# Kernel tuning notes

Hardware: AMD Instinct MI355X
Metric: run time of the kernel (lower is better)

The kernel has to match this reference:

```python
import jax, jax.numpy as jnp
import numpy as np

D, NH, K, FF, S, B = 256, 4, 1024, 1024, 2048, 4  # nhead*d_model must equal key_feature_dim=1024


def _ln(x, g, b, eps=1e-5):
    m = jnp.mean(x, axis=-1, keepdims=True)
    v = jnp.mean((x - m) ** 2, axis=-1, keepdims=True)
    return (x - m) / jnp.sqrt(v + eps) * g + b


def _l2norm(x, eps=1e-12):  # F.normalize(p=2, dim=-1)
    n = jnp.sqrt(jnp.sum(x * x, axis=-1, keepdims=True))
    return x / jnp.maximum(n, eps)


def setup_inputs() -> dict:
    key = jax.random.key(0)
    ks = jax.random.split(key, 16)
    def rn(i, shape, s):
        return jax.random.normal(ks[i], shape, jnp.float32) * jnp.float32(s)
    z = lambda shape: jnp.zeros(shape, jnp.float32)
    o = lambda shape: jnp.ones(shape, jnp.float32)
    return {
        "srcc": jax.random.normal(ks[0], (S, B, D), jnp.float32),
        "memory": jax.random.normal(ks[1], (S, B, D), jnp.float32),
        # per-head RelationUnit weights (stacked over NH heads)
        "WK": rn(2, (NH, K, D), np.sqrt(2.0 / K)),
        "WQ": rn(3, (NH, K, D), np.sqrt(2.0 / K)),
        "WV": rn(4, (NH, D, D), np.sqrt(2.0 / D)),
        "Wt": rn(5, (NH, D, D), np.sqrt(1.0 / D)),   # trans_conv
        # per-head TransNonlinear (extra_nonlinear)
        "e1w": rn(6, (NH, K, D), np.sqrt(1.0 / D)), "e1b": z((NH, K)),
        "e2w": rn(7, (NH, D, K), np.sqrt(1.0 / K)), "e2b": z((NH, D)),
        "eg": o((NH, D)), "eb": z((NH, D)),
        "Wout": rn(8, (D, NH * D), np.sqrt(1.0 / (NH * D))),  # trans_conv_out
        # decoder-layer FFN + norms
        "l1w": rn(9, (FF, D), np.sqrt(1.0 / D)), "l1b": z((FF,)),
        "l2w": rn(10, (D, FF), np.sqrt(1.0 / FF)), "l2b": z((D,)),
        "n1g": o((D,)), "n1b": z((D,)),
        "n3g": o((D,)), "n3b": z((D,)),
    }


def _forward(srcc, memory, WK, WQ, WV, Wt, e1w, e1b, e2w, e2b, eg, eb,
             Wout, l1w, l1b, l2w, l2b, n1g, n1b, n3g, n3b):
    # RMA(query=memory, key=srcc, value=srcc); dropout = identity (eval mode)
    q, kv = memory, srcc  # [S,B,D]
    wk = _l2norm(jnp.einsum('sbd,hkd->hsbk', kv, WK))   # [h,S,B,K]
    wq = _l2norm(jnp.einsum('sbd,hkd->hsbk', q, WQ))
    dot = jnp.einsum('hqbk,hsbk->hbqs', wq, wk)          # [h,B,Sq,Sk]
    aff = jax.nn.softmax(dot, axis=-1)
    # custom renormalization over the *query* axis (torch dim=1 of [B,Sq,Sk])
    aff = aff / (1e-9 + jnp.sum(aff, axis=2, keepdims=True))
    wv = jnp.einsum('sbd,hed->hbse', kv, WV)             # [h,B,Sk,D]
    o = jnp.einsum('hbqs,hbse->hqbe', aff, wv)           # [h,Sq,B,D]
    ru = jax.nn.relu(jnp.einsum('hqbd,hed->hqbe', q[None] - o, Wt))
    # per-head TransNonlinear
    hmid = jax.nn.relu(jnp.einsum('hqbd,hkd->hqbk', ru, e1w) + e1b[:, None, None, :])
    s2 = jnp.einsum('hqbk,hdk->hqbd', hmid, e2w) + e2b[:, None, None, :]
    xh = _ln(ru + s2, eg[:, None, None, :], eb[:, None, None, :])  # [h,S,B,D]
    cat = jnp.moveaxis(xh, 0, 2).reshape(q.shape[0], q.shape[1], NH * D)  # concat heads
    rma_out = jnp.einsum('sbk,dk->sbd', cat, Wout)       # [S,B,D]
    # decoder layer: note the faithful `[0]` indexing from the source
    srcc2 = rma_out[0]                                    # [B,D]
    x = _ln(memory + srcc2[None, :, :], n1g, n1b)         # broadcast residual
    ff = jax.nn.relu(x @ l1w.T + l1b) @ l2w.T + l2b
    return _ln(x + ff, n3g, n3b)


def reference(srcc, memory, WK, WQ, WV, Wt, e1w, e1b, e2w, e2b, eg, eb,
              Wout, l1w, l1b, l2w, l2b, n1g, n1b, n3g, n3b):
    return _forward(srcc, memory, WK, WQ, WV, Wt, e1w, e1b, e2w, e2b, eg, eb,
                    Wout, l1w, l1b, l2w, l2b, n1g, n1b, n3g, n3b)
```

## Files before the change

### kernel.cpp

```cpp
#include <hip/hip_runtime.h>
#include <stdint.h>
#include <stdio.h>

#define S_  2048
#define B_  4
#define D_  256
#define NH_ 4
#define K_  1024
#define FF_ 1024
#define M_  (S_*B_)
#define HB_ (NH_*B_)

#define LDSROW 136
#define PROW 144

typedef float  f32x4  __attribute__((ext_vector_type(4)));
typedef __bf16 bf16x8 __attribute__((ext_vector_type(8)));

__device__ __forceinline__ float bf2f(unsigned short u) {
  union { unsigned int i; float f; } v; v.i = ((unsigned int)u) << 16; return v.f;
}
__device__ __forceinline__ unsigned short f2bf(float f) {
  union { float f; unsigned int i; } v; v.f = f;
  unsigned int r = v.i + 0x7fffu + ((v.i >> 16) & 1u);
  return (unsigned short)(r >> 16);
}
__device__ __forceinline__ unsigned char f2fp8(float f) {
  return (unsigned char)(__builtin_amdgcn_cvt_pk_fp8_f32(f, f, 0, false) & 0xff);
}

__device__ __forceinline__ int kperm(int k) {
  int ks = k >> 5, quad = (k >> 3) & 3, b = k & 7;
  return ((ks >> 1) << 6) + (quad << 4) + ((ks & 1) << 3) + b;
}

__device__ __forceinline__ void gld_lds16(const void* g, void* l) {
  __builtin_amdgcn_global_load_lds(
      (__attribute__((address_space(1))) void*)(uintptr_t)g,
      (__attribute__((address_space(3))) void*)(uintptr_t)l, 16, 0, 0);
}

__device__ __forceinline__ void gemm_kloop(
    const unsigned short* __restrict__ Ag, const unsigned short* __restrict__ Bg,
    int lda, int ldb, int kdim,
    unsigned short* __restrict__ smA, unsigned short* __restrict__ smB,
    f32x4 acc[4][4])
{
  const int t    = threadIdx.x;
  const int wave = t >> 6;
  const int lane = t & 63;
  const int wm   = (wave >> 1) << 6;
  const int wn   = (wave & 1) << 6;
  const int c16  = lane & 15;
  const int quad = lane >> 4;

  for (int kc = 0; kc < kdim; kc += 64) {
    __syncthreads();
#pragma unroll
    for (int it = 0; it < 4; ++it) {
      int c   = it*256 + t;
      int row = c >> 3;
      int g   = (c & 7) ^ (row & 7);
      const unsigned short* ga = Ag + (size_t)row*lda + kc + g*8;
      const unsigned short* gb = Bg + (size_t)row*ldb + kc + g*8;
      unsigned short* la = smA + (size_t)(it*256 + wave*64)*8;
      unsigned short* lb = smB + (size_t)(it*256 + wave*64)*8;
      gld_lds16(ga, la);
      gld_lds16(gb, lb);
    }
    asm volatile("s_waitcnt vmcnt(0)" ::: "memory");
    __syncthreads();
#pragma unroll
    for (int ks = 0; ks < 2; ++ks) {
      bf16x8 av[4], bv[4];
#pragma unroll
      for (int i = 0; i < 4; ++i) {
        int ra = wm + i*16 + c16;
        av[i] = *(const bf16x8*)(smA + ra*64 + (((ks*4 + quad) ^ (ra & 7)))*8);
        int rb = wn + i*16 + c16;
        bv[i] = *(const bf16x8*)(smB + rb*64 + (((ks*4 + quad) ^ (rb & 7)))*8);
      }
#pragma unroll
      for (int i = 0; i < 4; ++i)
#pragma unroll
        for (int j = 0; j < 4; ++j)
          acc[i][j] = __builtin_amdgcn_mfma_f32_16x16x32_bf16(av[i], bv[j], acc[i][j], 0, 0, 0);
    }
  }
}

__device__ __forceinline__ float blk_sum256(float v, float* red) {
#pragma unroll
  for (int o = 32; o; o >>= 1) v += __shfl_xor(v, o, 64);
  __syncthreads();
  if ((threadIdx.x & 63) == 0) red[threadIdx.x >> 6] = v;
  __syncthreads();
  return red[0] + red[1] + red[2] + red[3];
}

__device__ __forceinline__ float wave_red(float a) {
#pragma unroll
  for (int o = 1; o < 64; o <<= 1) a += __shfl_xor(a, o, 64);
  return a;
}

__global__ void __launch_bounds__(256) k_cvt6(
    const float* __restrict__ s0, unsigned short* __restrict__ d0,
    const float* __restrict__ s1, unsigned short* __restrict__ d1,
    const float* __restrict__ s2, unsigned short* __restrict__ d2,
    const float* __restrict__ s3, unsigned short* __restrict__ d3,
    const float* __restrict__ s4, unsigned short* __restrict__ d4,
    const float* __restrict__ s5, unsigned short* __restrict__ d5) {
  int b = blockIdx.x;
  const float* src; unsigned short* dst; int base;
  if      (b < 2048) { src = s0; dst = d0; base = b; }
  else if (b < 4096) { src = s1; dst = d1; base = b - 2048; }
  else if (b < 5120) { src = s2; dst = d2; base = b - 4096; }
  else if (b < 6144) { src = s3; dst = d3; base = b - 5120; }
  else if (b < 6400) { src = s4; dst = d4; base = b - 6144; }
  else               { src = s5; dst = d5; base = b - 6400; }
  int i = (base*256 + threadIdx.x)*4;
  float4 v = *(const float4*)(src + i);
  ushort4 o;
  o.x = f2bf(v.x); o.y = f2bf(v.y); o.z = f2bf(v.z); o.w = f2bf(v.w);
  *(ushort4*)(dst + i) = o;
}

__global__ void __launch_bounds__(256) k_proj2(
    const unsigned short* __restrict__ X0, const unsigned short* __restrict__ W0,
    float* __restrict__ n0p, unsigned char* __restrict__ o0p,
    const unsigned short* __restrict__ X1, const unsigned short* __restrict__ W1,
    float* __restrict__ n1p, unsigned char* __restrict__ o1p) {
  __shared__ __align__(16) unsigned short sm[128*LDSROW];
  int which = blockIdx.x >> 11;
  const unsigned short* X = which ? X1 : X0;
  const unsigned short* W = which ? W1 : W0;
  float* nsq = which ? n1p : n0p;
  unsigned char* outp = which ? o1p : o0p;
  int l = blockIdx.x & 2047, x = l & 7, rblk = l >> 3;
  int m0 = (rblk >> 2)*128;
  int n0 = (x*4 + (rblk & 3))*128;
  f32x4 acc[4][4];
#pragma unroll
  for (int i = 0; i < 4; ++i)
#pragma unroll
    for (int j = 0; j < 4; ++j) acc[i][j] = f32x4{0.f,0.f,0.f,0.f};
  gemm_kloop(X + (size_t)m0*D_, W + (size_t)n0*D_, D_, D_, D_, sm, sm + 128*64, acc);
  const int t = threadIdx.x, wave = t>>6, lane = t&63;
  const int wm = (wave>>1)*64, wn = (wave&1)*64, quad = lane>>4, c16 = lane&15;
  const int h = n0 >> 10;
  unsigned char* sm8 = (unsigned char*)sm;
  __syncthreads();
#pragma unroll
  for (int i = 0; i < 4; ++i)
#pragma unroll
    for (int r = 0; r < 4; ++r) {
      int mloc = wm + i*16 + quad*4 + r;
      float sq = 0.f;
#pragma unroll
      for (int j = 0; j < 4; ++j) {
        float v = acc[i][j][r];
        sm8[mloc*PROW + kperm(wn + j*16 + c16)] = f2fp8(v);
        sq += v*v;
      }
      sq += __shfl_xor(sq, 1, 64); sq += __shfl_xor(sq, 2, 64);
      sq += __shfl_xor(sq, 4, 64); sq += __shfl_xor(sq, 8, 64);
      if (c16 == 0) {
        int m = m0 + mloc;
        atomicAdd(&nsq[(size_t)(h*B_ + (m & 3))*S_ + (m >> 2)], sq);
      }
    }
  __syncthreads();
  const int cg = t & 7, rsub = t >> 3;
#pragma unroll
  for (int c = 0; c < 4; ++c) {
    int mloc = c*32 + rsub;
    int m = m0 + mloc, s = m >> 2, b = m & 3;
    uint4 val = *(const uint4*)(sm8 + mloc*PROW + cg*16);
    *(uint4*)(outp + ((size_t)(h*B_ + b)*S_ + s)*K_ + (n0 & (K_-1)) + cg*16) = val;
  }
}

__global__ void __launch_bounds__(256) k_qkA(const unsigned char* __restrict__ wqa,
    const unsigned char* __restrict__ wka, const float* __restrict__ nq,
    const float* __restrict__ nk, float* __restrict__ lrow,
    unsigned short* __restrict__ E) {
  __shared__ __align__(16) unsigned short sm[128*LDSROW];
  unsigned char* smA = (unsigned char*)sm;
  unsigned char* smB = smA + 128*128;
  int l = blockIdx.x, x = l & 7, rblk = l >> 3;
  int hb = rblk >> 5;
  int rr = rblk & 31;
  int q0 = (x*2 + (rr & 1))*128;
  int s0 = (rr >> 1)*128;
  const unsigned char* A  = wqa + (size_t)hb*S_*K_ + (size_t)q0*K_;
  const unsigned char* Bm = wka + (size_t)hb*S_*K_ + (size_t)s0*K_;
  const int t = threadIdx.x, wave = t>>6, lane = t&63;
  const int wm = (wave>>1)*64, wn = (wave&1)*64, quad = lane>>4, c16 = lane&15;
  f32x4 acc[4][4];
#pragma unroll
  for (int i = 0; i < 4; ++i)
#pragma unroll
    for (int j = 0; j < 4; ++j) acc[i][j] = f32x4{0.f,0.f,0.f,0.f};

  for (int kc = 0; kc < K_; kc += 128) {
    __syncthreads();
#pragma unroll
    for (int it = 0; it < 4; ++it) {
      int c   = it*256 + t;
      int row = c >> 3;
      int g   = (c & 7) ^ (row & 7);
      gld_lds16(A  + (size_t)row*K_ + kc + g*16, smA + (size_t)(it*256 + wave*64)*16);
      gld_lds16(Bm + (size_t)row*K_ + kc + g*16, smB + (size_t)(it*256 + wave*64)*16);
    }
    asm volatile("s_waitcnt vmcnt(0)" ::: "memory");
    __syncthreads();
#pragma unroll
    for (int j2 = 0; j2 < 2; ++j2) {
      uint4 a4[4], b4[4];
#pragma unroll
      for (int i = 0; i < 4; ++i) {
        int ra = wm + i*16 + c16;
        a4[i] = *(const uint4*)(smA + ra*128 + (((j2*4 + quad) ^ (ra & 7)))*16);
        int rb = wn + i*16 + c16;
        b4[i] = *(const uint4*)(smB + rb*128 + (((j2*4 + quad) ^ (rb & 7)))*16);
      }
#pragma unroll
      for (int hh = 0; hh < 2; ++hh)
#pragma unroll
        for (int i = 0; i < 4; ++i)
#pragma unroll
          for (int j = 0; j < 4; ++j)
            acc[i][j] = __builtin_amdgcn_mfma_f32_16x16x32_fp8_fp8(
                ((const long*)&a4[i])[hh], ((const long*)&b4[j])[hh],
                acc[i][j], 0, 0, 0);
    }
  }

  float rk4[4];
#pragma unroll
  for (int j = 0; j < 4; ++j)
    rk4[j] = rsqrtf(nk[(size_t)hb*S_ + s0 + wn + j*16 + c16]);
  __syncthreads();
#pragma unroll
  for (int i = 0; i < 4; ++i)
#pragma unroll
    for (int r = 0; r < 4; ++r) {
      int qloc = wm + i*16 + quad*4 + r;
      float rq = rsqrtf(nq[(size_t)hb*S_ + q0 + qloc]);
      float rs = 0.f;
#pragma unroll
      for (int j = 0; j < 4; ++j) {
        float e = __expf(acc[i][j][r] * rq * rk4[j]);
        rs += e;
        sm[qloc*LDSROW + wn + j*16 + c16] = f2bf(e);
      }
      rs += __shfl_xor(rs, 1, 64); rs += __shfl_xor(rs, 2, 64);
      rs += __shfl_xor(rs, 4, 64); rs += __shfl_xor(rs, 8, 64);
      if (c16 == 0) atomicAdd(&lrow[(size_t)hb*S_ + q0 + qloc], rs);
    }
  __syncthreads();
  const int col8 = (t & 15)*8, rsub = t >> 4;
#pragma unroll
  for (int c = 0; c < 8; ++c) {
    int qloc = c*16 + rsub;
    uint4 val = *(const uint4*)(sm + qloc*LDSROW + col8);
    *(uint4*)(E + ((size_t)hb*S_ + q0 + qloc)*S_ + s0 + col8) = val;
  }
}

__global__ void __launch_bounds__(256) k_colsumE(const unsigned short* __restrict__ E,
    const float* __restrict__ lrow, float* __restrict__ colsum,
    float* __restrict__ p0) {
  __shared__ float il[128];
  int hb = blockIdx.x, qc = blockIdx.y;
  int t  = threadIdx.x;
  if (t < 128) il[t] = 1.f / lrow[(size_t)hb*S_ + qc*128 + t];
  __syncthreads();
  const unsigned short* Eb = E + (size_t)hb*S_*S_ + (size_t)(qc*128)*S_ + t*8;
  float acc8[8] = {0,0,0,0,0,0,0,0};
  for (int qi = 0; qi < 128; ++qi) {
    uint4 u = *(const uint4*)(Eb + (size_t)qi*S_);
    float w = il[qi];
    unsigned int ws_[4] = {u.x, u.y, u.z, u.w};
    float v8[8];
#pragma unroll
    for (int k = 0; k < 4; ++k) {
      v8[2*k]   = bf2f((unsigned short)(ws_[k] & 0xffffu));
      v8[2*k+1] = bf2f((unsigned short)(ws_[k] >> 16));
    }
#pragma unroll
    for (int k = 0; k < 8; ++k) acc8[k] += v8[k] * w;
    if (qc == 0 && qi == 0) {
#pragma unroll
      for (int k = 0; k < 8; ++k) p0[(size_t)hb*S_ + t*8 + k] = v8[k] * w;
    }
  }
#pragma unroll
  for (int k = 0; k < 8; ++k)
    atomicAdd(&colsum[(size_t)hb*S_ + t*8 + k], acc8[k]);
}

__global__ void __launch_bounds__(256) k_mid0(const float* __restrict__ p0,
    const float* __restrict__ colsum, const float* __restrict__ kv,
    float* __restrict__ cbuf) {
  __shared__ float aff[128];
  int hb = blockIdx.x, sc = blockIdx.y;
  int b = hb & 3;
  int t = threadIdx.x;
  if (t < 128) {
    int s = sc*128 + t;
    aff[t] = p0[(size_t)hb*S_ + s] / (1e-9f + colsum[(size_t)hb*S_ + s]);
  }
  __syncthreads();
  float acc = 0.f;
#pragma unroll 4
  for (int i = 0; i < 128; ++i) {
    int s = sc*128 + i;
    acc += aff[i] * kv[((size_t)s*B_ + b)*D_ + t];
  }
  atomicAdd(&cbuf[hb*D_ + t], acc);
}

__global__ void __launch_bounds__(256) k_mid1a(const float* __restrict__ cbuf,
    const float* __restrict__ mem, const float* __restrict__ WV,
    const float* __restrict__ Wt, float* __restrict__ ruW) {
  __shared__ float cS[D_], qmo[D_];
  int hb = blockIdx.x, h = hb >> 2, b = hb & 3;
  int t = threadIdx.x, wave = t >> 6, lane = t & 63;
  cS[t] = cbuf[hb*D_ + t];
  __syncthreads();
  float4 cv = *(const float4*)(cS + lane*4);
  for (int rr = 0; rr < 64; ++rr) {
    int e = wave*64 + rr;
    float4 w = *(const float4*)(WV + ((size_t)h*D_ + e)*D_ + lane*4);
    float a = wave_red(cv.x*w.x + cv.y*w.y + cv.z*w.z + cv.w*w.w);
    if (lane == 0) qmo[e] = mem[(size_t)b*D_ + e] - a;
  }
  __syncthreads();
  float4 qv = *(const float4*)(qmo + lane*4);
  for (int rr = 0; rr < 64; ++rr) {
    int e = wave*64 + rr;
    float4 w = *(const float4*)(Wt + ((size_t)h*D_ + e)*D_ + lane*4);
    float a = wave_red(qv.x*w.x + qv.y*w.y + qv.z*w.z + qv.w*w.w);
    if (lane == 0) ruW[hb*D_ + e] = fmaxf(a, 0.f);
  }
}

__global__ void __launch_bounds__(256) k_mid1b(const float* __restrict__ ruW,
    const float* __restrict__ e1w, const float* __restrict__ e1b,
    float* __restrict__ hmW) {
  __shared__ float ru[D_];
  int hb = blockIdx.x, kc = blockIdx.y, h = hb >> 2;
  int t = threadIdx.x, wave = t >> 6, lane = t & 63;
  ru[t] = ruW[hb*D_ + t];
  __syncthreads();
  float4 rv = *(const float4*)(ru + lane*4);
  for (int rr = 0; rr < 32; ++rr) {
    int k = kc*128 + wave*32 + rr;
    float4 w = *(const float4*)(e1w + ((size_t)h*K_ + k)*D_ + lane*4);
    float a = wave_red(rv.x*w.x + rv.y*w.y + rv.z*w.z + rv.w*w.w);
    if (lane == 0) hmW[hb*K_ + k] = fmaxf(a + e1b[(size_t)h*K_ + k], 0.f);
  }
}

__global__ void __launch_bounds__(256) k_mid1c(const float* __restrict__ hmW,
    const float* __restrict__ e2w, const float* __restrict__ e2b,
    float* __restrict__ s2W) {
  __shared__ float hm[K_];
  int hb = blockIdx.x, dc = blockIdx.y, h = hb >> 2;
  int t = threadIdx.x, wave = t >> 6, lane = t & 63;
  for (int k = t; k < K_; k += 256) hm[k] = hmW[hb*K_ + k];
  __syncthreads();
  for (int rr = 0; rr < 8; ++rr) {
    int d = dc*32 + wave*8 + rr;
    const float* row = e2w + ((size_t)h*D_ + d)*K_;
    float a = 0.f;
#pragma unroll
    for (int p = 0; p < 4; ++p) {
      float4 w = *(const float4*)(row + (p*64 + lane)*4);
      float4 hv = *(const float4*)(hm + (p*64 + lane)*4);
      a += w.x*hv.x + w.y*hv.y + w.z*hv.z + w.w*hv.w;
    }
    a = wave_red(a);
    if (lane == 0) s2W[hb*D_ + d] = a + e2b[(size_t)h*D_ + d];
  }
}

__global__ void __launch_bounds__(256) k_mid1d(const float* __restrict__ ruW,
    const float* __restrict__ s2W, const float* __restrict__ eg,
    const float* __restrict__ ebias, float* __restrict__ xh0) {
  __shared__ float red[4];
  int hb = blockIdx.x, h = hb >> 2;
  int t = threadIdx.x;
  float tv = ruW[hb*D_ + t] + s2W[hb*D_ + t];
  float mean = blk_sum256(tv, red) * (1.f/D_);
  float dv = tv - mean;
  float var = blk_sum256(dv*dv, red) * (1.f/D_);
  xh0[hb*D_ + t] = dv * rsqrtf(var + 1e-5f) * eg[(size_t)h*D_ + t] + ebias[(size_t)h*D_ + t];
}

__global__ void __launch_bounds__(256) k_mid2(const float* __restrict__ xh0,
    const float* __restrict__ Wout, float* __restrict__ srcc2) {
  __shared__ float cat[NH_*D_];
  int b = blockIdx.x, dc = blockIdx.y;
  int t = threadIdx.x, wave = t >> 6, lane = t & 63;
  for (int n = t; n < NH_*D_; n += 256)
    cat[n] = xh0[((size_t)(n >> 8)*B_ + b)*D_ + (n & 255)];
  __syncthreads();
  for (int rr = 0; rr < 8; ++rr) {
    int d = dc*32 + wave*8 + rr;
    const float* row = Wout + (size_t)d*(NH_*D_);
    float a = 0.f;
#pragma unroll
    for (int p = 0; p < 4; ++p) {
      float4 w = *(const float4*)(row + (p*64 + lane)*4);
      float4 cv = *(const float4*)(cat + (p*64 + lane)*4);
      a += w.x*cv.x + w.y*cv.y + w.z*cv.z + w.w*cv.w;
    }
    a = wave_red(a);
    if (lane == 0) srcc2[b*D_ + d] = a;
  }
}

__global__ void __launch_bounds__(256) k_f1(const float* __restrict__ mem,
    const float* __restrict__ srcc2, const float* __restrict__ g,
    const float* __restrict__ bb, float* __restrict__ xf,
    unsigned short* __restrict__ xb) {
  __shared__ float red[4];
  int m = blockIdx.x, t = threadIdx.x;
  float v = mem[(size_t)m*D_ + t] + srcc2[(m & 3)*D_ + t];
  float mean = blk_sum256(v, red) * (1.f/D_);
  float d = v - mean;
  float var = blk_sum256(d*d, red) * (1.f/D_);
  float y = d * rsqrtf(var + 1e-5f) * g[t] + bb[t];
  xf[(size_t)m*D_ + t] = y;
  xb[(size_t)m*D_ + t] = f2bf(y);
}

__global__ void __launch_bounds__(256) k_f2(const unsigned short* __restrict__ xb,
    const unsigned short* __restrict__ l1wb, const float* __restrict__ l1b,
    unsigned short* __restrict__ h1) {
  __shared__ __align__(16) unsigned short sm[128*LDSROW];
  int l = blockIdx.x;
  int n0 = (l & 7)*128, m0 = (l >> 3)*128;
  f32x4 acc[4][4];
#pragma unroll
  for (int i = 0; i < 4; ++i)
#pragma unroll
    for (int j = 0; j < 4; ++j) acc[i][j] = f32x4{0.f,0.f,0.f,0.f};
  gemm_kloop(xb + (size_t)m0*D_, l1wb + (size_t)n0*D_, D_, D_, D_, sm, sm + 128*64, acc);
  const int t = threadIdx.x, wave = t>>6, lane = t&63;
  const int wm = (wave>>1)*64, wn = (wave&1)*64, quad = lane>>4, c16 = lane&15;
  __syncthreads();
#pragma unroll
  for (int i = 0; i < 4; ++i)
#pragma unroll
    for (int r = 0; r < 4; ++r) {
      int mloc = wm + i*16 + quad*4 + r;
#pragma unroll
      for (int j = 0; j < 4; ++j) {
        int n = n0 + wn + j*16 + c16;
        sm[mloc*LDSROW + wn + j*16 + c16] = f2bf(fmaxf(acc[i][j][r] + l1b[n], 0.f));
      }
    }
  __syncthreads();
  const int col8 = (t & 15)*8, rsub = t >> 4;
#pragma unroll
  for (int c = 0; c < 8; ++c) {
    int mloc = c*16 + rsub;
    uint4 val = *(const uint4*)(sm + mloc*LDSROW + col8);
    *(uint4*)(h1 + (size_t)(m0 + mloc)*FF_ + n0 + col8) = val;
  }
}

__global__ void __launch_bounds__(256) k_f3(const unsigned short* __restrict__ h1,
    const unsigned short* __restrict__ l2wb, float* __restrict__ yf) {
  __shared__ __align__(16) unsigned short smA[128*64], smB[128*64];
  int l = blockIdx.x;
  int z = l & 1, n0 = ((l >> 1) & 1)*128, m0 = (l >> 2)*128;
  f32x4 acc[4][4];
#pragma unroll
  for (int i = 0; i < 4; ++i)
#pragma unroll
    for (int j = 0; j < 4; ++j) acc[i][j] = f32x4{0.f,0.f,0.f,0.f};
  gemm_kloop(h1 + (size_t)m0*FF_ + z*512, l2wb + (size_t)n0*FF_ + z*512,
             FF_, FF_, 512, smA, smB, acc);
  const int t = threadIdx.x, wave = t>>6, lane = t&63;
  const int wm = (wave>>1)*64, wn = (wave&1)*64, quad = lane>>4, c16 = lane&15;
#pragma unroll
  for (int i = 0; i < 4; ++i)
#pragma unroll
    for (int r = 0; r < 4; ++r) {
      int m = m0 + wm + i*16 + quad*4 + r;
#pragma unroll
      for (int j = 0; j < 4; ++j) {
        int n = n0 + wn + j*16 + c16;
        atomicAdd(&yf[(size_t)m*D_ + n], acc[i][j][r]);
      }
    }
}

__global__ void __launch_bounds__(256) k_f4(const float* __restrict__ yf,
    const float* __restrict__ l2b, const float* __restrict__ xf,
    const float* __restrict__ g, const float* __restrict__ bb,
    float* __restrict__ out) {
  __shared__ float red[4];
  int m = blockIdx.x, t = threadIdx.x;
  float v = yf[(size_t)m*D_ + t] + l2b[t] + xf[(size_t)m*D_ + t];
  float mean = blk_sum256(v, red) * (1.f/D_);
  float d = v - mean;
  float var = blk_sum256(d*d, red) * (1.f/D_);
  out[(size_t)m*D_ + t] = d * rsqrtf(var + 1e-5f) * g[t] + bb[t];
}

constexpr size_t SZ_ACT  = (size_t)HB_*S_*K_;
constexpr size_t OFF_WQA = 0;
constexpr size_t OFF_WKA = OFF_WQA + SZ_ACT;
constexpr size_t OFF_KVB = OFF_WKA + SZ_ACT;
constexpr size_t OFF_QB  = OFF_KVB + (size_t)M_*D_*2;
constexpr size_t OFF_WKW = OFF_QB  + (size_t)M_*D_*2;
constexpr size_t OFF_WQW = OFF_WKW + (size_t)NH_*K_*D_*2;
constexpr size_t OFF_L1W = OFF_WQW + (size_t)NH_*K_*D_*2;
constexpr size_t OFF_L2W = OFF_L1W + (size_t)FF_*D_*2;
constexpr size_t OFF_XB  = OFF_L2W + (size_t)D_*FF_*2;
constexpr size_t OFF_H1  = OFF_XB  + (size_t)M_*D_*2;
constexpr size_t OFF_XF  = OFF_H1  + (size_t)M_*FF_*2;
constexpr size_t OFF_YF  = OFF_XF  + (size_t)M_*D_*4;
constexpr size_t OFF_NQ  = OFF_YF  + (size_t)M_*D_*4;
constexpr size_t OFF_NK  = OFF_NQ + (size_t)HB_*S_*4;
constexpr size_t OFF_L   = OFF_NK + (size_t)HB_*S_*4;
constexpr size_t OFF_CS  = OFF_L  + (size_t)HB_*S_*4;
constexpr size_t OFF_CB  = OFF_CS + (size_t)HB_*S_*4;
constexpr size_t ZERO_BYTES = (size_t)HB_*S_*4*4 + (size_t)HB_*D_*4;
constexpr size_t OFF_P0  = OFF_CB + (size_t)HB_*D_*4;
constexpr size_t OFF_XH0 = OFF_P0 + (size_t)HB_*S_*4;
constexpr size_t OFF_SC2 = OFF_XH0 + (size_t)HB_*D_*4;
constexpr size_t OFF_RU  = OFF_SC2 + (size_t)B_*D_*4;
constexpr size_t OFF_HM  = OFF_RU  + (size_t)HB_*D_*4;
constexpr size_t OFF_S2  = OFF_HM  + (size_t)HB_*K_*4;
constexpr size_t OFF_E   = OFF_S2  + (size_t)HB_*D_*4;
constexpr size_t SZ_E    = (size_t)HB_*S_*S_*2;
constexpr size_t NEED_ALL = OFF_E + SZ_E;

extern "C" void kernel_launch(void* const* d_in, const int* in_sizes, int n_in,
                              void* d_out, int out_size, void* d_ws, size_t ws_size,
                              hipStream_t stream) {
  (void)in_sizes; (void)out_size;
  if (n_in < 21) return;
  const float* srcc = (const float*)d_in[0];
  const float* mem  = (const float*)d_in[1];
  const float* WK   = (const float*)d_in[2];
  const float* WQ   = (const float*)d_in[3];
  const float* WV   = (const float*)d_in[4];
  const float* Wt   = (const float*)d_in[5];
  const float* e1w  = (const float*)d_in[6];
  const float* e1b  = (const float*)d_in[7];
  const float* e2w  = (const float*)d_in[8];
  const float* e2b  = (const float*)d_in[9];
  const float* eg   = (const float*)d_in[10];
  const float* eb   = (const float*)d_in[11];
  const float* Wout = (const float*)d_in[12];
  const float* l1w  = (const float*)d_in[13];
  const float* l1b  = (const float*)d_in[14];
  const float* l2w  = (const float*)d_in[15];
  const float* l2b  = (const float*)d_in[16];
  const float* n1g  = (const float*)d_in[17];
  const float* n1b  = (const float*)d_in[18];
  const float* n3g  = (const float*)d_in[19];
  const float* n3b  = (const float*)d_in[20];

  char* ws = (char*)d_ws;
  if (ws_size < NEED_ALL) {
    fprintf(stderr, "kernel_launch: ws_size=%zu < required %zu bytes — aborting\n",
            ws_size, NEED_ALL);
    return;
  }

  unsigned char*  wqa  = (unsigned char*)(ws + OFF_WQA);
  unsigned char*  wka  = (unsigned char*)(ws + OFF_WKA);
  unsigned short* kvb  = (unsigned short*)(ws + OFF_KVB);
  unsigned short* qb   = (unsigned short*)(ws + OFF_QB);
  unsigned short* wkw  = (unsigned short*)(ws + OFF_WKW);
  unsigned short* wqw  = (unsigned short*)(ws + OFF_WQW);
  unsigned short* l1wb = (unsigned short*)(ws + OFF_L1W);
  unsigned short* l2wb = (unsigned short*)(ws + OFF_L2W);
  unsigned short* xb   = (unsigned short*)(ws + OFF_XB);
  unsigned short* h1   = (unsigned short*)(ws + OFF_H1);
  float* xf    = (float*)(ws + OFF_XF);
  float* yf    = (float*)(ws + OFF_YF);
  float* nq    = (float*)(ws + OFF_NQ);
  float* nk    = (float*)(ws + OFF_NK);
  float* lrow  = (float*)(ws + OFF_L);
  float* cs    = (float*)(ws + OFF_CS);
  float* cbuf  = (float*)(ws + OFF_CB);
  float* p0    = (float*)(ws + OFF_P0);
  float* xh0   = (float*)(ws + OFF_XH0);
  float* sc2   = (float*)(ws + OFF_SC2);
  float* ruW   = (float*)(ws + OFF_RU);
  float* hmW   = (float*)(ws + OFF_HM);
  float* s2W   = (float*)(ws + OFF_S2);
  unsigned short* E = (unsigned short*)(ws + OFF_E);

  hipMemsetAsync(ws + OFF_NQ, 0, ZERO_BYTES, stream);
  hipMemsetAsync(ws + OFF_YF, 0, (size_t)M_*D_*4, stream);

  k_cvt6<<<6656, 256, 0, stream>>>(srcc, kvb, mem, qb, WK, wkw, WQ, wqw,
                                   l1w, l1wb, l2w, l2wb);

  k_proj2<<<4096, 256, 0, stream>>>(kvb, wkw, nk, wka, qb, wqw, nq, wqa);

  k_qkA<<<4096, 256, 0, stream>>>(wqa, wka, nq, nk, lrow, E);
  k_colsumE<<<dim3(HB_, 16), 256, 0, stream>>>(E, lrow, cs, p0);

  k_mid0<<<dim3(HB_, S_/128), 256, 0, stream>>>(p0, cs, srcc, cbuf);
  k_mid1a<<<HB_, 256, 0, stream>>>(cbuf, mem, WV, Wt, ruW);
  k_mid1b<<<dim3(HB_, 8), 256, 0, stream>>>(ruW, e1w, e1b, hmW);
  k_mid1c<<<dim3(HB_, 8), 256, 0, stream>>>(hmW, e2w, e2b, s2W);
  k_mid1d<<<HB_, 256, 0, stream>>>(ruW, s2W, eg, eb, xh0);
  k_mid2<<<dim3(B_, 8), 256, 0, stream>>>(xh0, Wout, sc2);

  k_f1<<<M_, 256, 0, stream>>>(mem, sc2, n1g, n1b, xf, xb);
  k_f2<<<512, 256, 0, stream>>>(xb, l1wb, l1b, h1);
  k_f3<<<256, 256, 0, stream>>>(h1, l2wb, yf);
  k_f4<<<M_, 256, 0, stream>>>(yf, l2b, xf, n3g, n3b, (float*)d_out);
}
```

Before: 641.2 us.

## Store exp-score matrix in fp8, remap qkA blocks, split FFN2 partials

The unnormalised exponentiated score matrix E is stored as fp8 instead of bf16, which halves its write traffic in k_qkA and its read traffic in k_colsumE, where it is now decoded with packed fp8-to-f32 conversions. The block-to-tile mapping in k_qkA is reordered so that consecutive blocks share a head-batch and sweep query tiles, which may change cache reuse of the K operand. The FFN second GEMM writes its two K-split halves to separate buffers instead of using atomics, and the final LayerNorm sums them, which removes a memset. Storing E in fp8 lowers the precision of the attention weights.

After: 587.9 us. 1.09x faster.

```diff
diff --git a/kernel.cpp b/kernel.cpp
--- a/kernel.cpp
+++ b/kernel.cpp
@@ -15,6 +15,7 @@
 #define PROW 144
 
 typedef float  f32x4  __attribute__((ext_vector_type(4)));
+typedef float  f32x2  __attribute__((ext_vector_type(2)));
 typedef __bf16 bf16x8 __attribute__((ext_vector_type(8)));
 
 __device__ __forceinline__ float bf2f(unsigned short u) {
@@ -184,15 +185,15 @@
 __global__ void __launch_bounds__(256) k_qkA(const unsigned char* __restrict__ wqa,
     const unsigned char* __restrict__ wka, const float* __restrict__ nq,
     const float* __restrict__ nk, float* __restrict__ lrow,
-    unsigned short* __restrict__ E) {
+    unsigned char* __restrict__ E) {
   __shared__ __align__(16) unsigned short sm[128*LDSROW];
   unsigned char* smA = (unsigned char*)sm;
   unsigned char* smB = smA + 128*128;
   int l = blockIdx.x, x = l & 7, rblk = l >> 3;
-  int hb = rblk >> 5;
-  int rr = rblk & 31;
-  int q0 = (x*2 + (rr & 1))*128;
-  int s0 = (rr >> 1)*128;
+  int hb = x*2 + (rblk >> 8);
+  int r2 = rblk & 255;
+  int s0 = (r2 >> 4)*128;
+  int q0 = (r2 & 15)*128;
   const unsigned char* A  = wqa + (size_t)hb*S_*K_ + (size_t)q0*K_;
   const unsigned char* Bm = wka + (size_t)hb*S_*K_ + (size_t)s0*K_;
   const int t = threadIdx.x, wave = t>>6, lane = t&63;
@@ -241,6 +242,7 @@
 #pragma unroll
   for (int j = 0; j < 4; ++j)
     rk4[j] = rsqrtf(nk[(size_t)hb*S_ + s0 + wn + j*16 + c16]);
+  unsigned char* sm8 = (unsigned char*)sm;
   __syncthreads();
 #pragma unroll
   for (int i = 0; i < 4; ++i)
@@ -253,23 +255,23 @@
       for (int j = 0; j < 4; ++j) {
         float e = __expf(acc[i][j][r] * rq * rk4[j]);
         rs += e;
-        sm[qloc*LDSROW + wn + j*16 + c16] = f2bf(e);
+        sm8[qloc*PROW + wn + j*16 + c16] = f2fp8(e);
       }
       rs += __shfl_xor(rs, 1, 64); rs += __shfl_xor(rs, 2, 64);
       rs += __shfl_xor(rs, 4, 64); rs += __shfl_xor(rs, 8, 64);
       if (c16 == 0) atomicAdd(&lrow[(size_t)hb*S_ + q0 + qloc], rs);
     }
   __syncthreads();
-  const int col8 = (t & 15)*8, rsub = t >> 4;
-#pragma unroll
-  for (int c = 0; c < 8; ++c) {
-    int qloc = c*16 + rsub;
-    uint4 val = *(const uint4*)(sm + qloc*LDSROW + col8);
-    *(uint4*)(E + ((size_t)hb*S_ + q0 + qloc)*S_ + s0 + col8) = val;
-  }
-}
-
-__global__ void __launch_bounds__(256) k_colsumE(const unsigned short* __restrict__ E,
+  const int cg = t & 7, rsub = t >> 3;
+#pragma unroll
+  for (int c = 0; c < 4; ++c) {
+    int qloc = c*32 + rsub;
+    uint4 val = *(const uint4*)(sm8 + qloc*PROW + cg*16);
+    *(uint4*)(E + ((size_t)hb*S_ + q0 + qloc)*S_ + s0 + cg*16) = val;
+  }
+}
+
+__global__ void __launch_bounds__(256) k_colsumE(const unsigned char* __restrict__ E,
     const float* __restrict__ lrow, float* __restrict__ colsum,
     float* __restrict__ p0) {
   __shared__ float il[128];
@@ -277,18 +279,16 @@
   int t  = threadIdx.x;
   if (t < 128) il[t] = 1.f / lrow[(size_t)hb*S_ + qc*128 + t];
   __syncthreads();
-  const unsigned short* Eb = E + (size_t)hb*S_*S_ + (size_t)(qc*128)*S_ + t*8;
+  const unsigned char* Eb = E + (size_t)hb*S_*S_ + (size_t)(qc*128)*S_ + t*8;
   float acc8[8] = {0,0,0,0,0,0,0,0};
   for (int qi = 0; qi < 128; ++qi) {
-    uint4 u = *(const uint4*)(Eb + (size_t)qi*S_);
+    uint2 u = *(const uint2*)(Eb + (size_t)qi*S_);
     float w = il[qi];
-    unsigned int ws_[4] = {u.x, u.y, u.z, u.w};
-    float v8[8];
-#pragma unroll
-    for (int k = 0; k < 4; ++k) {
-      v8[2*k]   = bf2f((unsigned short)(ws_[k] & 0xffffu));
-      v8[2*k+1] = bf2f((unsigned short)(ws_[k] >> 16));
-    }
+    f32x2 v01 = __builtin_amdgcn_cvt_pk_f32_fp8(u.x, false);
+    f32x2 v23 = __builtin_amdgcn_cvt_pk_f32_fp8(u.x, true);
+    f32x2 v45 = __builtin_amdgcn_cvt_pk_f32_fp8(u.y, false);
+    f32x2 v67 = __builtin_amdgcn_cvt_pk_f32_fp8(u.y, true);
+    float v8[8] = {v01.x, v01.y, v23.x, v23.y, v45.x, v45.y, v67.x, v67.y};
 #pragma unroll
     for (int k = 0; k < 8; ++k) acc8[k] += v8[k] * w;
     if (qc == 0 && qi == 0) {
@@ -475,10 +475,12 @@
 }
 
 __global__ void __launch_bounds__(256) k_f3(const unsigned short* __restrict__ h1,
-    const unsigned short* __restrict__ l2wb, float* __restrict__ yf) {
+    const unsigned short* __restrict__ l2wb, float* __restrict__ yfa,
+    float* __restrict__ yfb) {
   __shared__ __align__(16) unsigned short smA[128*64], smB[128*64];
   int l = blockIdx.x;
   int z = l & 1, n0 = ((l >> 1) & 1)*128, m0 = (l >> 2)*128;
+  float* dst = z ? yfb : yfa;
   f32x4 acc[4][4];
 #pragma unroll
   for (int i = 0; i < 4; ++i)
@@ -496,18 +498,18 @@
 #pragma unroll
       for (int j = 0; j < 4; ++j) {
         int n = n0 + wn + j*16 + c16;
-        atomicAdd(&yf[(size_t)m*D_ + n], acc[i][j][r]);
+        dst[(size_t)m*D_ + n] = acc[i][j][r];
       }
     }
 }
 
-__global__ void __launch_bounds__(256) k_f4(const float* __restrict__ yf,
-    const float* __restrict__ l2b, const float* __restrict__ xf,
-    const float* __restrict__ g, const float* __restrict__ bb,
-    float* __restrict__ out) {
+__global__ void __launch_bounds__(256) k_f4(const float* __restrict__ yfa,
+    const float* __restrict__ yfb, const float* __restrict__ l2b,
+    const float* __restrict__ xf, const float* __restrict__ g,
+    const float* __restrict__ bb, float* __restrict__ out) {
   __shared__ float red[4];
   int m = blockIdx.x, t = threadIdx.x;
-  float v = yf[(size_t)m*D_ + t] + l2b[t] + xf[(size_t)m*D_ + t];
+  float v = yfa[(size_t)m*D_ + t] + yfb[(size_t)m*D_ + t] + l2b[t] + xf[(size_t)m*D_ + t];
   float mean = blk_sum256(v, red) * (1.f/D_);
   float d = v - mean;
   float var = blk_sum256(d*d, red) * (1.f/D_);
@@ -527,7 +529,8 @@
 constexpr size_t OFF_H1  = OFF_XB  + (size_t)M_*D_*2;
 constexpr size_t OFF_XF  = OFF_H1  + (size_t)M_*FF_*2;
 constexpr size_t OFF_YF  = OFF_XF  + (size_t)M_*D_*4;
-constexpr size_t OFF_NQ  = OFF_YF  + (size_t)M_*D_*4;
+constexpr size_t OFF_YF2 = OFF_YF  + (size_t)M_*D_*4;
+constexpr size_t OFF_NQ  = OFF_YF2 + (size_t)M_*D_*4;
 constexpr size_t OFF_NK  = OFF_NQ + (size_t)HB_*S_*4;
 constexpr size_t OFF_L   = OFF_NK + (size_t)HB_*S_*4;
 constexpr size_t OFF_CS  = OFF_L  + (size_t)HB_*S_*4;
@@ -540,7 +543,7 @@
 constexpr size_t OFF_HM  = OFF_RU  + (size_t)HB_*D_*4;
 constexpr size_t OFF_S2  = OFF_HM  + (size_t)HB_*K_*4;
 constexpr size_t OFF_E   = OFF_S2  + (size_t)HB_*D_*4;
-constexpr size_t SZ_E    = (size_t)HB_*S_*S_*2;
+constexpr size_t SZ_E    = (size_t)HB_*S_*S_;
 constexpr size_t NEED_ALL = OFF_E + SZ_E;
 
 extern "C" void kernel_launch(void* const* d_in, const int* in_sizes, int n_in,
@@ -589,6 +592,7 @@
   unsigned short* h1   = (unsigned short*)(ws + OFF_H1);
   float* xf    = (float*)(ws + OFF_XF);
   float* yf    = (float*)(ws + OFF_YF);
+  float* yf2   = (float*)(ws + OFF_YF2);
   float* nq    = (float*)(ws + OFF_NQ);
   float* nk    = (float*)(ws + OFF_NK);
   float* lrow  = (float*)(ws + OFF_L);
@@ -600,10 +604,9 @@
   float* ruW   = (float*)(ws + OFF_RU);
   float* hmW   = (float*)(ws + OFF_HM);
   float* s2W   = (float*)(ws + OFF_S2);
-  unsigned short* E = (unsigned short*)(ws + OFF_E);
+  unsigned char* E = (unsigned char*)(ws + OFF_E);
 
   hipMemsetAsync(ws + OFF_NQ, 0, ZERO_BYTES, stream);
-  hipMemsetAsync(ws + OFF_YF, 0, (size_t)M_*D_*4, stream);
 
   k_cvt6<<<6656, 256, 0, stream>>>(srcc, kvb, mem, qb, WK, wkw, WQ, wqw,
                                    l1w, l1wb, l2w, l2wb);
@@ -622,6 +625,6 @@
 
   k_f1<<<M_, 256, 0, stream>>>(mem, sc2, n1g, n1b, xf, xb);
   k_f2<<<512, 256, 0, stream>>>(xb, l1wb, l1b, h1);
-  k_f3<<<256, 256, 0, stream>>>(h1, l2wb, yf);
-  k_f4<<<M_, 256, 0, stream>>>(yf, l2b, xf, n3g, n3b, (float*)d_out);
-}
+  k_f3<<<256, 256, 0, stream>>>(h1, l2wb, yf, yf2);
+  k_f4<<<M_, 256, 0, stream>>>(yf, yf2, l2b, xf, n3g, n3b, (float*)d_out);
+}
```
